# Optimization experiments

Measured on AMD Instinct MI355X. Metric: run time of the kernel, lower is better.

Reference implementation:

```python
import jax, jax.numpy as jnp
import numpy as np

EMBED_DIM = 1024
NUM_HEADS = 16
HEAD_DIM = EMBED_DIM // NUM_HEADS


def setup_inputs() -> dict:
    key = jax.random.key(0)
    k1, k2, k3, k4, k5 = jax.random.split(key, 5)
    B, S, E = 2, 2048, EMBED_DIM
    scale = 1.0 / np.sqrt(E)
    return {
        "query": jax.random.normal(k1, (B, S, E), dtype=jnp.float32),
        "W_qkv": jax.random.normal(k2, (E, 3 * E), dtype=jnp.float32) * scale,
        "b_qkv": jnp.zeros((3 * E,), dtype=jnp.float32),
        "W_out": jax.random.normal(k3, (E, E), dtype=jnp.float32) * scale,
        "b_out": jnp.zeros((E,), dtype=jnp.float32),
    }


def reference(query, W_qkv, b_qkv, W_out, b_out):
    B, S, E = query.shape
    H, D = NUM_HEADS, HEAD_DIM
    # Fused QKV projection: [B,S,3E] -> [B,S,3,H,D]
    qkv = (query @ W_qkv + b_qkv).reshape(B, S, 3, H, D)
    q, k, v = qkv[:, :, 0], qkv[:, :, 1], qkv[:, :, 2]  # each [B,S,H,D]
    # Scores: [B,H,S,S]
    scores = jnp.einsum("bqhd,bkhd->bhqk", q, k) / np.sqrt(D).astype(query.dtype)
    attn = jax.nn.softmax(scores, axis=-1)
    # Dropout is identity in eval mode.
    out = jnp.einsum("bhqk,bkhd->bqhd", attn, v).reshape(B, S, E)
    return out @ W_out + b_out
```

## Files before the change

### kernel.cpp

```cpp
#include <hip/hip_runtime.h>
#include <stdint.h>

typedef __attribute__((ext_vector_type(4))) float f32x4;
typedef __attribute__((ext_vector_type(16))) float f32x16;
typedef __attribute__((ext_vector_type(8))) __bf16 bf16x8;
typedef __attribute__((ext_vector_type(2))) unsigned int u32v2;

#define GLDS(g, s) __builtin_amdgcn_global_load_lds( \
    (const __attribute__((address_space(1))) void*)(g), \
    (__attribute__((address_space(3))) void*)(s), 16, 0, 0)

#define SWZ8(r) ((((r) ^ ((r) >> 3))) & 7)

__device__ inline float fast_exp2(float x){
#if __has_builtin(__builtin_amdgcn_exp2f)
  return __builtin_amdgcn_exp2f(x);
#else
  float r; asm("v_exp_f32 %0, %1" : "=v"(r) : "v"(x)); return r;
#endif
}

__device__ inline unsigned short f2bf(float f){
  union { float f; unsigned int u; } v; v.f = f;
  unsigned int u = v.u;
  unsigned int r = (u + 0x7fffu + ((u >> 16) & 1u)) >> 16;
  return (unsigned short)r;
}

__global__ __launch_bounds__(256) void prep(const float* __restrict__ x,
                                            const float* __restrict__ Wqkv,
                                            const float* __restrict__ Wout,
                                            unsigned short* __restrict__ y,
                                            unsigned short* __restrict__ wqkvT,
                                            unsigned short* __restrict__ woutT){
  __shared__ float tile[64][65];
  const int bx = blockIdx.x;
  const int t = threadIdx.x;
  if (bx < 2048){
    const size_t i = ((size_t)bx * 256 + t) * 8;
    float4 a = *reinterpret_cast<const float4*>(x + i);
    float4 b = *reinterpret_cast<const float4*>(x + i + 4);
    uint4 o;
    o.x = (unsigned)f2bf(a.x) | ((unsigned)f2bf(a.y) << 16);
    o.y = (unsigned)f2bf(a.z) | ((unsigned)f2bf(a.w) << 16);
    o.z = (unsigned)f2bf(b.x) | ((unsigned)f2bf(b.y) << 16);
    o.w = (unsigned)f2bf(b.z) | ((unsigned)f2bf(b.w) << 16);
    *reinterpret_cast<uint4*>(y + i) = o;
    return;
  }
  const int tb = bx - 2048;
  const int nb = tb & 63;
  const int k0 = (tb >> 6) * 64;
  const float* W; unsigned short* WT; int N, n0;
  if (nb < 48){ W = Wqkv; WT = wqkvT; N = 3072; n0 = nb * 64; }
  else        { W = Wout; WT = woutT; N = 1024; n0 = (nb - 48) * 64; }
  #pragma unroll
  for (int p = 0; p < 16; p++){
    int idx = p * 256 + t; int r = idx >> 6, c = idx & 63;
    tile[r][c] = W[(size_t)(k0 + r) * N + n0 + c];
  }
  __syncthreads();
  #pragma unroll
  for (int p = 0; p < 16; p++){
    int idx = p * 256 + t; int r = idx >> 6, c = idx & 63;
    WT[(size_t)(n0 + r) * 1024 + k0 + c] = f2bf(tile[c][r]);
  }
}

template<int MODE>
__global__ __launch_bounds__(256) void gemm_bt(
    const unsigned short* __restrict__ X,
    const unsigned short* __restrict__ WT,
    const float* __restrict__ bias,
    unsigned short* __restrict__ oq,
    unsigned short* __restrict__ ok,
    unsigned short* __restrict__ ovt,
    float* __restrict__ ofp)
{
  constexpr int Kdim = 1024;
  constexpr int BN = (MODE == 0) ? 128 : 64;
  constexpr int JN = (MODE == 0) ? 4 : 2;
  __shared__ __align__(16) unsigned short As[128 * 32];
  __shared__ __align__(16) unsigned short Bs[BN * 32];
  const int t  = threadIdx.x;
  const int l  = t & 63;
  const int w  = t >> 6;
  const int lr = l & 15, lg = l >> 4;
  const int wr = w >> 1, wc = w & 1;

  const unsigned nx = gridDim.x;
  const unsigned nwg = nx * gridDim.y;
  const unsigned f0 = blockIdx.y * nx + blockIdx.x;
  const unsigned f  = (f0 & 7) * (nwg >> 3) + (f0 >> 3);
  const int m0 = (int)(f / nx) * 128;
  const int n0 = (int)(f % nx) * BN;

  const int lrow = l >> 2;
  const int lch  = (l & 3) * 8;
  const unsigned short* gA0 = X  + (size_t)(m0 + w * 16 + lrow) * Kdim + lch;
  const unsigned short* gA1 = gA0 + (size_t)64 * Kdim;
  const unsigned short* gB0 = WT + (size_t)(n0 + w * 16 + lrow) * Kdim + lch;
  unsigned short* lA0 = &As[(w * 16) * 32];
  unsigned short* lA1 = &As[(64 + w * 16) * 32];
  unsigned short* lB0 = &Bs[(w * 16) * 32];

  f32x4 zero4 = {0.f, 0.f, 0.f, 0.f};
  f32x4 acc[4][JN];
  #pragma unroll
  for (int i = 0; i < 4; i++)
    #pragma unroll
    for (int j = 0; j < JN; j++) acc[i][j] = zero4;

  const int aoff = (wr * 64 + lr) * 32 + lg * 8;
  const int boff = (wc * (BN / 2) + lr) * 32 + lg * 8;

  for (int kt = 0; kt < Kdim / 32; ++kt){
    const int kb = kt * 32;
    __syncthreads();
    GLDS(gA0 + kb, lA0);
    GLDS(gA1 + kb, lA1);
    GLDS(gB0 + kb, lB0);
    if constexpr (MODE == 0){
      const unsigned short* gB1 = gB0 + (size_t)64 * Kdim;
      GLDS(gB1 + kb, &Bs[(64 + w * 16) * 32]);
    }
    __syncthreads();
    bf16x8 af[4], bfr[JN];
    #pragma unroll
    for (int i = 0; i < 4; i++)  af[i]  = *reinterpret_cast<const bf16x8*>(&As[aoff + i * 16 * 32]);
    #pragma unroll
    for (int j = 0; j < JN; j++) bfr[j] = *reinterpret_cast<const bf16x8*>(&Bs[boff + j * 16 * 32]);
    __builtin_amdgcn_s_setprio(1);
    #pragma unroll
    for (int i = 0; i < 4; i++)
      #pragma unroll
      for (int j = 0; j < JN; j++)
        acc[i][j] = __builtin_amdgcn_mfma_f32_16x16x32_bf16(af[i], bfr[j], acc[i][j], 0, 0, 0);
    __builtin_amdgcn_s_setprio(0);
  }

  const int mbg = m0 + wr * 64;
  const int nb  = n0 + wc * (BN / 2);
  if constexpr (MODE == 0){
    __shared__ __align__(16) unsigned short Ep[4][64 * 72];
    unsigned short* E = Ep[w];
    const int which = n0 >> 10;
    const int h = (nb >> 6) & 15;
    const float qs = (which == 0) ? 0.18033688011f : 1.0f;
    #pragma unroll
    for (int j = 0; j < 4; j++){
      const float bs = bias[nb + j * 16 + lr];
      const int nloc = j * 16 + lr;
      #pragma unroll
      for (int i = 0; i < 4; i++){
        #pragma unroll
        for (int r = 0; r < 4; r++){
          const int mloc = i * 16 + 4 * lg + r;
          const unsigned short vv = f2bf((acc[i][j][r] + bs) * qs);
          if (which == 2) E[nloc * 72 + mloc] = vv;
          else            E[mloc * 72 + nloc] = vv;
        }
      }
    }
    asm volatile("s_waitcnt lgkmcnt(0)" ::: "memory");
    __builtin_amdgcn_sched_barrier(0);
    const int b = mbg >> 11, sib = mbg & 2047;
    const size_t bh = (size_t)(b * 16 + h);
    if (which == 2){
      unsigned short* dst = ovt + bh * 64 * 2048 + sib;
      #pragma unroll
      for (int it = 0; it < 8; ++it){
        const int d = it * 8 + (l >> 3);
        const int sc8 = (l & 7) * 8;
        uint4 xv = *reinterpret_cast<const uint4*>(&E[d * 72 + sc8]);
        *reinterpret_cast<uint4*>(dst + (size_t)d * 2048 + sc8) = xv;
      }
    } else {
      unsigned short* dst = (which == 0 ? oq : ok) + (bh * 2048 + sib) * 64;
      #pragma unroll
      for (int it = 0; it < 8; ++it){
        const int sl = it * 8 + (l >> 3);
        const int dc8 = (l & 7) * 8;
        uint4 xv = *reinterpret_cast<const uint4*>(&E[sl * 72 + dc8]);
        *reinterpret_cast<uint4*>(dst + (size_t)sl * 64 + dc8) = xv;
      }
    }
  } else {
    __shared__ __align__(16) float Epf[4][64 * 36];
    float* E = Epf[w];
    #pragma unroll
    for (int j = 0; j < JN; j++){
      const float bs = bias[nb + j * 16 + lr];
      const int nloc = j * 16 + lr;
      #pragma unroll
      for (int i = 0; i < 4; i++){
        #pragma unroll
        for (int r = 0; r < 4; r++){
          const int mloc = i * 16 + 4 * lg + r;
          E[mloc * 36 + nloc] = acc[i][j][r] + bs;
        }
      }
    }
    asm volatile("s_waitcnt lgkmcnt(0)" ::: "memory");
    __builtin_amdgcn_sched_barrier(0);
    #pragma unroll
    for (int it = 0; it < 8; ++it){
      const int ml = it * 8 + (l >> 3);
      const int nc = (l & 7) * 4;
      uint4 xv = *reinterpret_cast<const uint4*>(&E[ml * 36 + nc]);
      *reinterpret_cast<uint4*>(ofp + (size_t)(mbg + ml) * 1024 + nb + nc) = xv;
    }
  }
}

__global__ __launch_bounds__(256) void attn_fwd(
    const unsigned short* __restrict__ Q,
    const unsigned short* __restrict__ Kt,
    const unsigned short* __restrict__ VT,
    unsigned short* __restrict__ O)
{
  __shared__ __align__(16) unsigned short Ks[2][4096];
  __shared__ __align__(16) unsigned short Vs[2][4096];
  const int t = threadIdx.x;
  const int l = t & 63, w = t >> 6;
  const int q5 = l & 31;
  const int hi = l >> 5;

  const unsigned flat = blockIdx.y * gridDim.x + blockIdx.x;
  const unsigned fl = (flat & 7) * 64 + (flat >> 3);
  const int bh = fl >> 4;
  const int q0 = (fl & 15) * 128 + w * 32;

  const unsigned short* Qb = Q + ((size_t)bh * 2048 + q0) * 64;
  bf16x8 qf0 = *reinterpret_cast<const bf16x8*>(Qb + (size_t)q5 * 64 +  0 + hi * 8);
  bf16x8 qf1 = *reinterpret_cast<const bf16x8*>(Qb + (size_t)q5 * 64 + 16 + hi * 8);
  bf16x8 qf2 = *reinterpret_cast<const bf16x8*>(Qb + (size_t)q5 * 64 + 32 + hi * 8);
  bf16x8 qf3 = *reinterpret_cast<const bf16x8*>(Qb + (size_t)q5 * 64 + 48 + hi * 8);
  const unsigned short* Kb = Kt + (size_t)bh * 2048 * 64;
  const unsigned short* Vb = VT + (size_t)bh * 64 * 2048;

  union U8 { unsigned u[4]; uint4 u4; bf16x8 b; };

  const int r0 = t >> 3,        c0 = t & 7;
  const int r1 = 32 + (t >> 3), c1 = t & 7;
  const int kof0 = r0 * 64 + ((c0 ^ SWZ8(r0)) * 8);
  const int kof1 = r1 * 64 + ((c1 ^ SWZ8(r1)) * 8);
  const unsigned short* gK0 = Kb + r0 * 64 + c0 * 8;
  const unsigned short* gK1 = Kb + r1 * 64 + c1 * 8;
  const unsigned short* gV0 = Vb + (size_t)r0 * 2048 + c0 * 8;
  const unsigned short* gV1 = Vb + (size_t)r1 * 2048 + c1 * 8;

  uint4 pk0 = *reinterpret_cast<const uint4*>(gK0);
  uint4 pk1 = *reinterpret_cast<const uint4*>(gK1);
  uint4 pv0 = *reinterpret_cast<const uint4*>(gV0);
  uint4 pv1 = *reinterpret_cast<const uint4*>(gV1);

  float l_run = 0.f;
  f32x16 o40 = {}, o41 = {};
  const int row_lo = q5, row_hi = 32 + q5;
  const int swz_lo = SWZ8(row_lo), swz_hi = SWZ8(row_hi);

  for (int kt = 0; kt < 32; ++kt){
    const int cur = kt & 1;
    *reinterpret_cast<uint4*>(&Ks[cur][kof0]) = pk0;
    *reinterpret_cast<uint4*>(&Ks[cur][kof1]) = pk1;
    *reinterpret_cast<uint4*>(&Vs[cur][kof0]) = pv0;
    *reinterpret_cast<uint4*>(&Vs[cur][kof1]) = pv1;
    __syncthreads();
    if (kt < 31){
      pk0 = *reinterpret_cast<const uint4*>(gK0 + (kt + 1) * 4096);
      pk1 = *reinterpret_cast<const uint4*>(gK1 + (kt + 1) * 4096);
      pv0 = *reinterpret_cast<const uint4*>(gV0 + (kt + 1) * 64);
      pv1 = *reinterpret_cast<const uint4*>(gV1 + (kt + 1) * 64);
    }

    f32x16 sc0 = {}, sc1 = {};
    __builtin_amdgcn_s_setprio(1);
    #pragma unroll
    for (int ks = 0; ks < 4; ks++){
      const int ch = ks * 2 + hi;
      bf16x8 k0f = *reinterpret_cast<const bf16x8*>(&Ks[cur][row_lo * 64 + ((ch ^ swz_lo) * 8)]);
      bf16x8 k1f = *reinterpret_cast<const bf16x8*>(&Ks[cur][row_hi * 64 + ((ch ^ swz_hi) * 8)]);
      bf16x8 qk = (ks == 0) ? qf0 : (ks == 1) ? qf1 : (ks == 2) ? qf2 : qf3;
      sc0 = __builtin_amdgcn_mfma_f32_32x32x16_bf16(k0f, qk, sc0, 0, 0, 0);
      sc1 = __builtin_amdgcn_mfma_f32_32x32x16_bf16(k1f, qk, sc1, 0, 0, 0);
    }
    __builtin_amdgcn_s_setprio(0);

    float psum = 0.f;
    unsigned cw0[8], cw1[8];
    #pragma unroll
    for (int g = 0; g < 4; g++){
      float p0 = fast_exp2(sc0[4*g+0]);
      float p1 = fast_exp2(sc0[4*g+1]);
      float p2 = fast_exp2(sc0[4*g+2]);
      float p3 = fast_exp2(sc0[4*g+3]);
      psum += (p0 + p1) + (p2 + p3);
      asm("v_cvt_pk_bf16_f32 %0, %1, %2" : "=v"(cw0[2*g])   : "v"(p0), "v"(p1));
      asm("v_cvt_pk_bf16_f32 %0, %1, %2" : "=v"(cw0[2*g+1]) : "v"(p2), "v"(p3));
    }
    #pragma unroll
    for (int g = 0; g < 4; g++){
      float p0 = fast_exp2(sc1[4*g+0]);
      float p1 = fast_exp2(sc1[4*g+1]);
      float p2 = fast_exp2(sc1[4*g+2]);
      float p3 = fast_exp2(sc1[4*g+3]);
      psum += (p0 + p1) + (p2 + p3);
      asm("v_cvt_pk_bf16_f32 %0, %1, %2" : "=v"(cw1[2*g])   : "v"(p0), "v"(p1));
      asm("v_cvt_pk_bf16_f32 %0, %1, %2" : "=v"(cw1[2*g+1]) : "v"(p2), "v"(p3));
    }
    psum += __shfl_xor(psum, 32);
    l_run += psum;

    bf16x8 pb[4];
    #pragma unroll
    for (int ks = 0; ks < 4; ks++){
      const unsigned* cw = (ks < 2) ? cw0 : cw1;
      const int base = (ks & 1) * 4;
      const unsigned a = cw[base + 0], b2 = cw[base + 1];
      const unsigned c = cw[base + 2], d = cw[base + 3];
      u32v2 s1 = __builtin_amdgcn_permlane32_swap(a, c, false, false);
      u32v2 s2 = __builtin_amdgcn_permlane32_swap(b2, d, false, false);
      U8 pu;
      pu.u[0] = s1[0]; pu.u[1] = s2[0]; pu.u[2] = s1[1]; pu.u[3] = s2[1];
      pb[ks] = pu.b;
    }

    __builtin_amdgcn_s_setprio(1);
    #pragma unroll
    for (int ks = 0; ks < 4; ks++){
      const int ch = ks * 2 + hi;
      bf16x8 v0f = *reinterpret_cast<const bf16x8*>(&Vs[cur][row_lo * 64 + ((ch ^ swz_lo) * 8)]);
      bf16x8 v1f = *reinterpret_cast<const bf16x8*>(&Vs[cur][row_hi * 64 + ((ch ^ swz_hi) * 8)]);
      o40 = __builtin_amdgcn_mfma_f32_32x32x16_bf16(v0f, pb[ks], o40, 0, 0, 0);
      o41 = __builtin_amdgcn_mfma_f32_32x32x16_bf16(v1f, pb[ks], o41, 0, 0, 0);
    }
    __builtin_amdgcn_s_setprio(0);
  }

  __syncthreads();
  uint2* Eq = reinterpret_cast<uint2*>(&Ks[0][0]) + w * 512;
  const float rinv = 1.f / l_run;
  const int swzp = SWZ8(q5);
  #pragma unroll
  for (int g = 0; g < 4; g++){
    float a0 = o40[4*g+0] * rinv, a1 = o40[4*g+1] * rinv;
    float a2 = o40[4*g+2] * rinv, a3 = o40[4*g+3] * rinv;
    unsigned w0, w1;
    asm("v_cvt_pk_bf16_f32 %0, %1, %2" : "=v"(w0) : "v"(a0), "v"(a1));
    asm("v_cvt_pk_bf16_f32 %0, %1, %2" : "=v"(w1) : "v"(a2), "v"(a3));
    uint2 pkv; pkv.x = w0; pkv.y = w1;
    Eq[q5 * 16 + ((g ^ swzp) * 2) + hi] = pkv;
  }
  #pragma unroll
  for (int g = 0; g < 4; g++){
    float a0 = o41[4*g+0] * rinv, a1 = o41[4*g+1] * rinv;
    float a2 = o41[4*g+2] * rinv, a3 = o41[4*g+3] * rinv;
    unsigned w0, w1;
    asm("v_cvt_pk_bf16_f32 %0, %1, %2" : "=v"(w0) : "v"(a0), "v"(a1));
    asm("v_cvt_pk_bf16_f32 %0, %1, %2" : "=v"(w1) : "v"(a2), "v"(a3));
    uint2 pkv; pkv.x = w0; pkv.y = w1;
    Eq[q5 * 16 + (((4 + g) ^ swzp) * 2) + hi] = pkv;
  }
  const int qr = l >> 1;
  const int cbase = (l & 1) * 4;
  const int swzq = SWZ8(qr);
  const int b = bh >> 4, h = bh & 15;
  unsigned short* Ob = O + ((size_t)b * 2048 + q0 + qr) * 1024 + h * 64;
  #pragma unroll
  for (int cc = 0; cc < 4; ++cc){
    const int c = cbase + cc;
    const int base = qr * 16 + ((c ^ swzq) * 2);
    uint2 lo = Eq[base];
    uint2 hi2 = Eq[base + 1];
    uint4 xv; xv.x = lo.x; xv.y = lo.y; xv.z = hi2.x; xv.w = hi2.y;
    *reinterpret_cast<uint4*>(Ob + c * 8) = xv;
  }
}

extern "C" void kernel_launch(void* const* d_in, const int* in_sizes, int n_in,
                              void* d_out, int out_size, void* d_ws, size_t ws_size,
                              hipStream_t stream){
  const float* query = (const float*)d_in[0];
  const float* Wqkv  = (const float*)d_in[1];
  const float* bqkv  = (const float*)d_in[2];
  const float* Wout  = (const float*)d_in[3];
  const float* bout  = (const float*)d_in[4];
  float* out = (float*)d_out;

  unsigned short* ws    = (unsigned short*)d_ws;
  unsigned short* xbf   = ws;
  unsigned short* wqkvT = xbf   + 4194304;
  unsigned short* woutT = wqkvT + 3145728;
  unsigned short* qbf   = woutT + 1048576;
  unsigned short* kbf   = qbf   + 4194304;
  unsigned short* vtbf  = kbf   + 4194304;
  unsigned short* abf   = xbf;

  prep<<<3072, 256, 0, stream>>>(query, Wqkv, Wout, xbf, wqkvT, woutT);
  gemm_bt<0><<<dim3(24, 32), 256, 0, stream>>>(xbf, wqkvT, bqkv, qbf, kbf, vtbf, nullptr);
  attn_fwd<<<dim3(16, 32), 256, 0, stream>>>(qbf, kbf, vtbf, abf);
  gemm_bt<1><<<dim3(16, 32), 256, 0, stream>>>(abf, woutT, bout, nullptr, nullptr, nullptr, out);
}
```

Baseline: 128.5 us.

## Use K=64 tiles in QKV GEMM and alias epilogue staging onto shared LDS buffer

For the QKV projection GEMM (MODE 0), the K tile grows from 32 to 64, so each iteration does 32 MFMAs per wave with half as many barrier pairs and loop trips. The operand and epilogue shared-memory arrays are merged into one aliased buffer, with an added barrier before the epilogue. This cuts the LDS footprint, which can raise occupancy. The rows are unswizzled with a 64-element stride, which risks LDS bank conflicts on the fragment reads, and the larger tile uses more registers.

After: 141.8 us. 10.4% more time.

```diff
diff --git a/kernel.cpp b/kernel.cpp
--- a/kernel.cpp
+++ b/kernel.cpp
@@ -80,8 +80,7 @@
   constexpr int Kdim = 1024;
   constexpr int BN = (MODE == 0) ? 128 : 64;
   constexpr int JN = (MODE == 0) ? 4 : 2;
-  __shared__ __align__(16) unsigned short As[128 * 32];
-  __shared__ __align__(16) unsigned short Bs[BN * 32];
+  __shared__ __align__(16) unsigned short SMEM[18432];
   const int t  = threadIdx.x;
   const int l  = t & 63;
   const int w  = t >> 6;
@@ -95,15 +94,6 @@
   const int m0 = (int)(f / nx) * 128;
   const int n0 = (int)(f % nx) * BN;
 
-  const int lrow = l >> 2;
-  const int lch  = (l & 3) * 8;
-  const unsigned short* gA0 = X  + (size_t)(m0 + w * 16 + lrow) * Kdim + lch;
-  const unsigned short* gA1 = gA0 + (size_t)64 * Kdim;
-  const unsigned short* gB0 = WT + (size_t)(n0 + w * 16 + lrow) * Kdim + lch;
-  unsigned short* lA0 = &As[(w * 16) * 32];
-  unsigned short* lA1 = &As[(64 + w * 16) * 32];
-  unsigned short* lB0 = &Bs[(w * 16) * 32];
-
   f32x4 zero4 = {0.f, 0.f, 0.f, 0.f};
   f32x4 acc[4][JN];
   #pragma unroll
@@ -111,39 +101,93 @@
     #pragma unroll
     for (int j = 0; j < JN; j++) acc[i][j] = zero4;
 
-  const int aoff = (wr * 64 + lr) * 32 + lg * 8;
-  const int boff = (wc * (BN / 2) + lr) * 32 + lg * 8;
-
-  for (int kt = 0; kt < Kdim / 32; ++kt){
-    const int kb = kt * 32;
-    __syncthreads();
-    GLDS(gA0 + kb, lA0);
-    GLDS(gA1 + kb, lA1);
-    GLDS(gB0 + kb, lB0);
-    if constexpr (MODE == 0){
-      const unsigned short* gB1 = gB0 + (size_t)64 * Kdim;
-      GLDS(gB1 + kb, &Bs[(64 + w * 16) * 32]);
-    }
-    __syncthreads();
-    bf16x8 af[4], bfr[JN];
-    #pragma unroll
-    for (int i = 0; i < 4; i++)  af[i]  = *reinterpret_cast<const bf16x8*>(&As[aoff + i * 16 * 32]);
-    #pragma unroll
-    for (int j = 0; j < JN; j++) bfr[j] = *reinterpret_cast<const bf16x8*>(&Bs[boff + j * 16 * 32]);
-    __builtin_amdgcn_s_setprio(1);
-    #pragma unroll
-    for (int i = 0; i < 4; i++)
-      #pragma unroll
-      for (int j = 0; j < JN; j++)
-        acc[i][j] = __builtin_amdgcn_mfma_f32_16x16x32_bf16(af[i], bfr[j], acc[i][j], 0, 0, 0);
-    __builtin_amdgcn_s_setprio(0);
+  if constexpr (MODE == 0){
+    unsigned short* As = SMEM;
+    unsigned short* Bs = SMEM + 8192;
+    const int srow = l >> 3;
+    const int sch  = (l & 7) * 8;
+    const unsigned short* gA[4];
+    const unsigned short* gB[4];
+    unsigned short* lA[4];
+    unsigned short* lB[4];
+    #pragma unroll
+    for (int i = 0; i < 4; i++){
+      gA[i] = X  + (size_t)(m0 + w * 32 + i * 8 + srow) * Kdim + sch;
+      lA[i] = &As[(w * 32 + i * 8) * 64];
+      gB[i] = WT + (size_t)(n0 + w * 32 + i * 8 + srow) * Kdim + sch;
+      lB[i] = &Bs[(w * 32 + i * 8) * 64];
+    }
+    for (int kt = 0; kt < 16; ++kt){
+      const int kb = kt * 64;
+      __syncthreads();
+      #pragma unroll
+      for (int i = 0; i < 4; i++) GLDS(gA[i] + kb, lA[i]);
+      #pragma unroll
+      for (int i = 0; i < 4; i++) GLDS(gB[i] + kb, lB[i]);
+      __syncthreads();
+      bf16x8 af[4][2], bfr[4][2];
+      #pragma unroll
+      for (int i = 0; i < 4; i++){
+        const int ro = (wr * 64 + i * 16 + lr) * 64 + lg * 8;
+        af[i][0] = *reinterpret_cast<const bf16x8*>(&As[ro]);
+        af[i][1] = *reinterpret_cast<const bf16x8*>(&As[ro + 32]);
+      }
+      #pragma unroll
+      for (int j = 0; j < 4; j++){
+        const int ro = (wc * 64 + j * 16 + lr) * 64 + lg * 8;
+        bfr[j][0] = *reinterpret_cast<const bf16x8*>(&Bs[ro]);
+        bfr[j][1] = *reinterpret_cast<const bf16x8*>(&Bs[ro + 32]);
+      }
+      __builtin_amdgcn_s_setprio(1);
+      #pragma unroll
+      for (int i = 0; i < 4; i++)
+        #pragma unroll
+        for (int j = 0; j < 4; j++){
+          acc[i][j] = __builtin_amdgcn_mfma_f32_16x16x32_bf16(af[i][0], bfr[j][0], acc[i][j], 0, 0, 0);
+          acc[i][j] = __builtin_amdgcn_mfma_f32_16x16x32_bf16(af[i][1], bfr[j][1], acc[i][j], 0, 0, 0);
+        }
+      __builtin_amdgcn_s_setprio(0);
+    }
+  } else {
+    unsigned short* As = SMEM;
+    unsigned short* Bs = SMEM + 4096;
+    const int lrow = l >> 2;
+    const int lch  = (l & 3) * 8;
+    const unsigned short* gA0 = X  + (size_t)(m0 + w * 16 + lrow) * Kdim + lch;
+    const unsigned short* gA1 = gA0 + (size_t)64 * Kdim;
+    const unsigned short* gB0 = WT + (size_t)(n0 + w * 16 + lrow) * Kdim + lch;
+    unsigned short* lA0 = &As[(w * 16) * 32];
+    unsigned short* lA1 = &As[(64 + w * 16) * 32];
+    unsigned short* lB0 = &Bs[(w * 16) * 32];
+    const int aoff = (wr * 64 + lr) * 32 + lg * 8;
+    const int boff = (wc * 32 + lr) * 32 + lg * 8;
+    for (int kt = 0; kt < 32; ++kt){
+      const int kb = kt * 32;
+      __syncthreads();
+      GLDS(gA0 + kb, lA0);
+      GLDS(gA1 + kb, lA1);
+      GLDS(gB0 + kb, lB0);
+      __syncthreads();
+      bf16x8 af[4], bfr[2];
+      #pragma unroll
+      for (int i = 0; i < 4; i++)  af[i]  = *reinterpret_cast<const bf16x8*>(&As[aoff + i * 16 * 32]);
+      #pragma unroll
+      for (int j = 0; j < 2; j++) bfr[j] = *reinterpret_cast<const bf16x8*>(&Bs[boff + j * 16 * 32]);
+      __builtin_amdgcn_s_setprio(1);
+      #pragma unroll
+      for (int i = 0; i < 4; i++)
+        #pragma unroll
+        for (int j = 0; j < 2; j++)
+          acc[i][j] = __builtin_amdgcn_mfma_f32_16x16x32_bf16(af[i], bfr[j], acc[i][j], 0, 0, 0);
+      __builtin_amdgcn_s_setprio(0);
+    }
   }
 
   const int mbg = m0 + wr * 64;
   const int nb  = n0 + wc * (BN / 2);
+  __syncthreads();
   if constexpr (MODE == 0){
-    __shared__ __align__(16) unsigned short Ep[4][64 * 72];
-    unsigned short* E = Ep[w];
+    unsigned short* E = SMEM + w * 4608;
     const int which = n0 >> 10;
     const int h = (nb >> 6) & 15;
     const float qs = (which == 0) ? 0.18033688011f : 1.0f;
@@ -186,8 +230,7 @@
       }
     }
   } else {
-    __shared__ __align__(16) float Epf[4][64 * 36];
-    float* E = Epf[w];
+    float* E = reinterpret_cast<float*>(SMEM) + w * 2304;
     #pragma unroll
     for (int j = 0; j < JN; j++){
       const float bs = bias[nb + j * 16 + lr];
```
